# Kernel optimization log

Measured on AMD Instinct MI355X. Metric: run time of the kernel, lower is better.

The kernel has to match this reference:

```python
import jax, jax.numpy as jnp
import numpy as np

B, H, W, C = 16, 56, 56, 512
NUM_HEADS = 8
WS = 4  # window_size


def setup_inputs() -> dict:
    key = jax.random.key(0)
    k1, k2, k3, k4 = jax.random.split(key, 4)
    x = jax.random.normal(k1, (B, H, W, C), dtype=jnp.float32)
    w_qkv_h = jax.random.normal(k2, (3 * C, C), dtype=jnp.float32) * 0.02
    w_qkv_l = jax.random.normal(k3, (3 * C, C), dtype=jnp.float32) * 0.02
    w_proj = jax.random.normal(k4, (C, 2 * C), dtype=jnp.float32) * 0.02
    b_proj = jnp.zeros((C,), dtype=jnp.float32)
    return {"x": x, "w_qkv_h": w_qkv_h, "w_qkv_l": w_qkv_l,
            "w_proj": w_proj, "b_proj": b_proj}


def reference(x, w_qkv_h, w_qkv_l, w_proj, b_proj):
    b, h, w, c = x.shape
    nh = NUM_HEADS
    hd = c // nh
    nw = WS * WS  # tokens per window
    scale = c ** -0.5  # NOTE: original scales by full dim, not head dim

    # window partition: [B*H/ws*W/ws, ws*ws, C]
    xw = x.reshape(b, h // WS, WS, w // WS, WS, c)
    xw = xw.transpose(0, 1, 3, 2, 4, 5).reshape(-1, nw, c)

    # local branch qkv: [3, Nwin, nh, nw, hd]
    qkv_h = (xw @ w_qkv_h.T).reshape(-1, nw, 3, nh, hd).transpose(2, 0, 3, 1, 4)
    q_h, k_h, v_h = qkv_h[0], qkv_h[1], qkv_h[2]

    # global branch: average-pool each window to a single token [Nwin, 1, C]
    x_avg = x.reshape(b, h // WS, WS, w // WS, WS, c).mean(axis=(2, 4))
    x_avg = x_avg.reshape(-1, 1, c)
    qkv_l = (x_avg @ w_qkv_l.T).reshape(-1, 1, 3, nh, hd).transpose(2, 0, 3, 1, 4)
    q_l, k_l, v_l = qkv_l[0], qkv_l[1], qkv_l[2]

    # local window attention: [Nwin, nh, nw, nw]
    attn_h = jax.nn.softmax(jnp.einsum('bhqd,bhkd->bhqk', q_h, k_h) * scale, axis=-1)
    x_h = jnp.einsum('bhqk,bhkd->bhqd', attn_h, v_h)
    x_h = x_h.transpose(0, 2, 1, 3).reshape(-1, nw, c)

    # pooled global attention (1 token -> softmax over singleton = 1)
    attn_l = jax.nn.softmax(jnp.einsum('bhqd,bhkd->bhqk', q_l, k_l) * scale, axis=-1)
    x_l = jnp.einsum('bhqk,bhkd->bhqd', attn_l, v_l)
    x_l = x_l.transpose(0, 2, 1, 3).reshape(-1, 1, c)

    # concat local + broadcast global, project 2C -> C
    x_out = jnp.concatenate([x_h, jnp.broadcast_to(x_l, (x_l.shape[0], nw, c))], axis=-1)
    x_out = x_out @ w_proj.T + b_proj

    # window reverse
    x_out = x_out.reshape(b, h // WS, w // WS, WS, WS, c)
    x_out = x_out.transpose(0, 1, 3, 2, 4, 5).reshape(b, h, w, c)
    return x_out
```

## Files before the change

kernel.cpp:

```cpp
#include <hip/hip_runtime.h>


using bf16x8 = __attribute__((ext_vector_type(8))) short;
using f32x4  = __attribute__((ext_vector_type(4))) float;

#define SCALE 0.044194173824159216f

__device__ __forceinline__ unsigned short f2bf(float f) {
    union { float f; unsigned u; } v; v.f = f;
    unsigned u = v.u;
    return (unsigned short)((u + 0x7fffu + ((u >> 16) & 1u)) >> 16);
}

__device__ __forceinline__ void gl2lds16(const unsigned short* g, unsigned short* l) {
    __builtin_amdgcn_global_load_lds(
        (const __attribute__((address_space(1))) void*)g,
        (__attribute__((address_space(3))) void*)l, 16, 0, 0);
}

__global__ void k_prep_weights(const float* __restrict__ wqkv_h,
                               const float* __restrict__ wqkv_l,
                               const float* __restrict__ wproj,
                               unsigned short* __restrict__ WH,
                               unsigned short* __restrict__ WLV,
                               unsigned short* __restrict__ WP1,
                               unsigned short* __restrict__ WP2) {
    int i = blockIdx.x * 256 + threadIdx.x;
    if (i < 786432) {
        WH[i] = f2bf(wqkv_h[i]);
    } else {
        int j = i - 786432;
        int r = j >> 18;
        int t = j & 262143;
        int n = t >> 9, k = t & 511;
        if (r == 0)      WLV[t] = f2bf(wqkv_l[(1024 + n) * 512 + k]);
        else if (r == 1) WP1[t] = f2bf(wproj[n * 1024 + k]);
        else             WP2[t] = f2bf(wproj[n * 1024 + 512 + k]);
    }
}

__global__ void k_window_pool(const float* __restrict__ x,
                              unsigned short* __restrict__ XW,
                              unsigned short* __restrict__ XAVG) {
    int win = blockIdx.x * 2 + (threadIdx.x >> 7);
    int g = threadIdx.x & 127;
    int c = g * 4;
    int b = win / 196, rem = win % 196, wh = rem / 14, ww = rem % 14;
    float4 s = {0.f, 0.f, 0.f, 0.f};
    #pragma unroll
    for (int t = 0; t < 16; ++t) {
        int row = (b * 56 + wh * 4 + (t >> 2)) * 56 + ww * 4 + (t & 3);
        float4 v = *(const float4*)&x[(size_t)row * 512 + c];
        uint2 pk;
        pk.x = (unsigned)f2bf(v.x) | ((unsigned)f2bf(v.y) << 16);
        pk.y = (unsigned)f2bf(v.z) | ((unsigned)f2bf(v.w) << 16);
        *(uint2*)&XW[(size_t)(win * 16 + t) * 512 + c] = pk;
        s.x += v.x; s.y += v.y; s.z += v.z; s.w += v.w;
    }
    uint2 pa;
    pa.x = (unsigned)f2bf(s.x * 0.0625f) | ((unsigned)f2bf(s.y * 0.0625f) << 16);
    pa.y = (unsigned)f2bf(s.z * 0.0625f) | ((unsigned)f2bf(s.w * 0.0625f) << 16);
    *(uint2*)&XAVG[(size_t)win * 512 + c] = pa;
}

template <int NT>
__global__ void k_gemm512(const unsigned short* __restrict__ A,
                          const unsigned short* __restrict__ Bw,
                          unsigned short* __restrict__ outB,
                          float* __restrict__ outF,
                          const float* __restrict__ bias) {
    int wave = threadIdx.x >> 6, lane = threadIdx.x & 63;
    int quad = lane >> 4, l16 = lane & 15;
    int m0 = blockIdx.x * 64 + wave * 16;
    int n0 = blockIdx.y * (NT * 16);
    f32x4 acc[NT] = {};
    const unsigned short* arow = A + (size_t)(m0 + l16) * 512 + quad * 8;
    for (int kk = 0; kk < 16; ++kk) {
        bf16x8 a = *(const bf16x8*)(arow + kk * 32);
        #pragma unroll
        for (int nt = 0; nt < NT; ++nt) {
            bf16x8 b = *(const bf16x8*)(Bw + (size_t)(n0 + nt * 16 + l16) * 512 + kk * 32 + quad * 8);
            acc[nt] = __builtin_amdgcn_mfma_f32_16x16x32_bf16(a, b, acc[nt], 0, 0, 0);
        }
    }
    #pragma unroll
    for (int nt = 0; nt < NT; ++nt) {
        int col = n0 + nt * 16 + l16;
        float bv = (bias != nullptr) ? bias[col] : 0.f;
        #pragma unroll
        for (int r = 0; r < 4; ++r) {
            int row = m0 + quad * 4 + r;
            if (outF != nullptr) outF[(size_t)row * 512 + col] = acc[nt][r] + bv;
            else                 outB[(size_t)row * 512 + col] = f2bf(acc[nt][r]);
        }
    }
}

__global__ void __launch_bounds__(256, 4) k_fused(const unsigned short* __restrict__ XW,
                                                  const unsigned short* __restrict__ WH,
                                                  unsigned short* __restrict__ XH) {
    __shared__ __align__(16) char smem[33792];
    unsigned short* As  = (unsigned short*)smem;
    unsigned short* Bs  = (unsigned short*)(smem + 8192);
    unsigned short* qs  = (unsigned short*)smem;
    unsigned short* ks  = (unsigned short*)(smem + 9216);
    unsigned short* vts = (unsigned short*)(smem + 18432);
    unsigned short* Ps  = (unsigned short*)(smem + 29696);

    const int wave = threadIdx.x >> 6, lane = threadIdx.x & 63;
    const int quad = lane >> 4, l16 = lane & 15;

    int id  = blockIdx.y * 784 + blockIdx.x;
    int s   = id >> 3;
    int tb  = (id & 7) * 98 + (s >> 3);
    int head = s & 7;
    const int m0 = tb * 64;
    const int t0 = wave * 16;
    const unsigned short* Bh = WH + head * 32768;

    int aofs[2], bofs[6];
    #pragma unroll
    for (int i = 0; i < 2; ++i) {
        int u = (wave * 2 + i) * 64 + lane;
        int n = u >> 3;
        int gu = (lane & 7) ^ (n & 7);
        aofs[i] = (m0 + n) * 512 + gu * 8;
    }
    #pragma unroll
    for (int i = 0; i < 6; ++i) {
        int u = (wave * 6 + i) * 64 + lane;
        int n = u >> 3;
        int gu = (lane & 7) ^ (n & 7);
        int nrow = (n >> 6) * 512 + (n & 63);
        bofs[i] = nrow * 512 + gu * 8;
    }

    f32x4 acc[4][3] = {};
    const int sx = l16 & 7;

    for (int ch = 0; ch < 8; ++ch) {
        #pragma unroll
        for (int i = 0; i < 2; ++i)
            gl2lds16(XW + aofs[i] + ch * 64, As + (wave * 2 + i) * 512);
        #pragma unroll
        for (int i = 0; i < 6; ++i)
            gl2lds16(Bh + bofs[i] + ch * 64, Bs + (wave * 6 + i) * 512);
        __syncthreads();
        #pragma unroll
        for (int kk = 0; kk < 2; ++kk) {
            int su = ((kk * 4 + quad) ^ sx) * 8;
            bf16x8 a[4], b[3];
            #pragma unroll
            for (int mf = 0; mf < 4; ++mf)
                a[mf] = *(const bf16x8*)&As[(mf * 16 + l16) * 64 + su];
            #pragma unroll
            for (int j = 0; j < 3; ++j)
                b[j] = *(const bf16x8*)&Bs[(wave * 48 + j * 16 + l16) * 64 + su];
            #pragma unroll
            for (int mf = 0; mf < 4; ++mf)
                #pragma unroll
                for (int j = 0; j < 3; ++j)
                    acc[mf][j] = __builtin_amdgcn_mfma_f32_16x16x32_bf16(a[mf], b[j], acc[mf][j], 0, 0, 0);
        }
        __syncthreads();
    }

    #pragma unroll
    for (int j = 0; j < 3; ++j) {
        int cb = wave * 48 + j * 16;
        #pragma unroll
        for (int mf = 0; mf < 4; ++mf) {
            #pragma unroll
            for (int r = 0; r < 4; ++r) {
                int tok = mf * 16 + quad * 4 + r;
                unsigned short hv = f2bf(acc[mf][j][r]);
                if (cb < 64)       qs[tok * 72 + cb + l16] = hv;
                else if (cb < 128) ks[tok * 72 + (cb - 64) + l16] = hv;
                else               vts[(cb - 128 + l16) * 88 + tok] = hv;
            }
        }
    }
    __syncthreads();

    if (wave == 3) {
        #pragma unroll
        for (int i = 0; i < 16; ++i) vts[lane * 88 + 64 + i] = 0;
    }
    {
        int prow = lane >> 2, pc = 16 + (lane & 3) * 4;
        #pragma unroll
        for (int i = 0; i < 4; ++i) Ps[wave * 512 + prow * 32 + pc + i] = 0;
    }

    f32x4 sacc = {};
    {
        bf16x8 a0 = *(const bf16x8*)&qs[(t0 + l16) * 72 + quad * 8];
        bf16x8 b0 = *(const bf16x8*)&ks[(t0 + l16) * 72 + quad * 8];
        sacc = __builtin_amdgcn_mfma_f32_16x16x32_bf16(a0, b0, sacc, 0, 0, 0);
        bf16x8 a1 = *(const bf16x8*)&qs[(t0 + l16) * 72 + 32 + quad * 8];
        bf16x8 b1 = *(const bf16x8*)&ks[(t0 + l16) * 72 + 32 + quad * 8];
        sacc = __builtin_amdgcn_mfma_f32_16x16x32_bf16(a1, b1, sacc, 0, 0, 0);
    }
    float p[4];
    #pragma unroll
    for (int r = 0; r < 4; ++r) {
        float v = sacc[r] * SCALE;
        float m = v;
        m = fmaxf(m, __shfl_xor(m, 1));
        m = fmaxf(m, __shfl_xor(m, 2));
        m = fmaxf(m, __shfl_xor(m, 4));
        m = fmaxf(m, __shfl_xor(m, 8));
        float e = __expf(v - m);
        float sm = e;
        sm += __shfl_xor(sm, 1);
        sm += __shfl_xor(sm, 2);
        sm += __shfl_xor(sm, 4);
        sm += __shfl_xor(sm, 8);
        p[r] = e / sm;
    }
    #pragma unroll
    for (int r = 0; r < 4; ++r)
        Ps[wave * 512 + (quad * 4 + r) * 32 + l16] = f2bf(p[r]);

    bf16x8 pa = *(const bf16x8*)&Ps[wave * 512 + l16 * 32 + quad * 8];
    #pragma unroll
    for (int nt = 0; nt < 4; ++nt) {
        f32x4 y = {};
        bf16x8 bv = *(const bf16x8*)&vts[(nt * 16 + l16) * 88 + t0 + quad * 8];
        y = __builtin_amdgcn_mfma_f32_16x16x32_bf16(pa, bv, y, 0, 0, 0);
        #pragma unroll
        for (int r = 0; r < 4; ++r)
            XH[(size_t)(m0 + t0 + quad * 4 + r) * 512 + head * 64 + nt * 16 + l16] = f2bf(y[r]);
    }
}

__global__ void __launch_bounds__(256, 3) k_gemm_proj(const unsigned short* __restrict__ XH,
                                                      const unsigned short* __restrict__ WP1,
                                                      const float* __restrict__ G,
                                                      float* __restrict__ out) {
    __shared__ __align__(16) unsigned short As[8192];
    __shared__ __align__(16) unsigned short Bs[8192];

    const int wave = threadIdx.x >> 6, lane = threadIdx.x & 63;
    const int quad = lane >> 4, l16 = lane & 15;

    int id = blockIdx.y * 392 + blockIdx.x;
    int s  = id >> 3;
    int xb = (id & 7) * 49 + (s >> 2);
    int yb = s & 3;
    const int m0 = xb * 128, n0 = yb * 128;
    const int wm = (wave >> 1) * 64;
    const int wn = (wave & 1) * 64;

    int aofs[4], bofs[4];
    #pragma unroll
    for (int i = 0; i < 4; ++i) {
        int u = (wave * 4 + i) * 64 + lane;
        int n = u >> 3;
        int gu = (lane & 7) ^ (n & 7);
        aofs[i] = (m0 + n) * 512 + gu * 8;
        bofs[i] = (n0 + n) * 512 + gu * 8;
    }

    f32x4 acc[4][4] = {};
    const int sx = l16 & 7;

    for (int ch = 0; ch < 8; ++ch) {
        #pragma unroll
        for (int i = 0; i < 4; ++i) {
            gl2lds16(XH + aofs[i] + ch * 64, As + (wave * 4 + i) * 512);
            gl2lds16(WP1 + bofs[i] + ch * 64, Bs + (wave * 4 + i) * 512);
        }
        __syncthreads();
        #pragma unroll
        for (int kk = 0; kk < 2; ++kk) {
            int su = ((kk * 4 + quad) ^ sx) * 8;
            bf16x8 a[4], b[4];
            #pragma unroll
            for (int mf = 0; mf < 4; ++mf)
                a[mf] = *(const bf16x8*)&As[(wm + mf * 16 + l16) * 64 + su];
            #pragma unroll
            for (int j = 0; j < 4; ++j)
                b[j] = *(const bf16x8*)&Bs[(wn + j * 16 + l16) * 64 + su];
            #pragma unroll
            for (int mf = 0; mf < 4; ++mf)
                #pragma unroll
                for (int j = 0; j < 4; ++j)
                    acc[mf][j] = __builtin_amdgcn_mfma_f32_16x16x32_bf16(a[mf], b[j], acc[mf][j], 0, 0, 0);
        }
        __syncthreads();
    }

    #pragma unroll
    for (int mf = 0; mf < 4; ++mf) {
        #pragma unroll
        for (int r = 0; r < 4; ++r) {
            int tl  = wm + mf * 16 + quad * 4 + r;
            int gt  = m0 + tl;
            int win = gt >> 4, tw = gt & 15;
            int bb = win / 196, rem = win % 196;
            int wh = rem / 14, ww = rem % 14;
            int orow = (bb * 56 + wh * 4 + (tw >> 2)) * 56 + ww * 4 + (tw & 3);
            #pragma unroll
            for (int j = 0; j < 4; ++j) {
                int ncol = n0 + wn + j * 16 + l16;
                out[(size_t)orow * 512 + ncol] = acc[mf][j][r] + G[(size_t)win * 512 + ncol];
            }
        }
    }
}

extern "C" void kernel_launch(void* const* d_in, const int* in_sizes, int n_in,
                              void* d_out, int out_size, void* d_ws, size_t ws_size,
                              hipStream_t stream) {
    const float* x      = (const float*)d_in[0];
    const float* wqkv_h = (const float*)d_in[1];
    const float* wqkv_l = (const float*)d_in[2];
    const float* wproj  = (const float*)d_in[3];
    const float* bproj  = (const float*)d_in[4];
    float* out = (float*)d_out;

    char* ws = (char*)d_ws;
    unsigned short* WH   = (unsigned short*)(ws + 0);
    unsigned short* WLV  = (unsigned short*)(ws + 1572864);
    unsigned short* WP1  = (unsigned short*)(ws + 2097152);
    unsigned short* WP2  = (unsigned short*)(ws + 2621440);
    unsigned short* XW   = (unsigned short*)(ws + 3145728);
    unsigned short* XAVG = (unsigned short*)(ws + 54525952);
    unsigned short* VL   = (unsigned short*)(ws + 57737216);
    float*          G    = (float*)(ws + 60948480);
    unsigned short* XH   = (unsigned short*)(ws + 67371008);

    k_prep_weights<<<dim3(6144), dim3(256), 0, stream>>>(wqkv_h, wqkv_l, wproj, WH, WLV, WP1, WP2);
    k_window_pool<<<dim3(1568), dim3(256), 0, stream>>>(x, XW, XAVG);
    k_gemm512<2><<<dim3(49, 16), dim3(256), 0, stream>>>(XAVG, WLV, VL, (float*)nullptr, (const float*)nullptr);
    k_gemm512<2><<<dim3(49, 16), dim3(256), 0, stream>>>(VL, WP2, (unsigned short*)nullptr, G, bproj);
    k_fused<<<dim3(784, 8), dim3(256), 0, stream>>>(XW, WH, XH);
    k_gemm_proj<<<dim3(392, 4), dim3(256), 0, stream>>>(XH, WP1, G, out);
}
```

Baseline: 386.6 us.

## Double-buffer LDS loads in fused attention and projection GEMMs, widen fused blocks

```diff
diff --git a/kernel.cpp b/kernel.cpp
--- a/kernel.cpp
+++ b/kernel.cpp
@@ -96,66 +96,84 @@
     }
 }
 
-__global__ void __launch_bounds__(256, 4) k_fused(const unsigned short* __restrict__ XW,
+__global__ void __launch_bounds__(512, 4) k_fused(const unsigned short* __restrict__ XW,
                                                   const unsigned short* __restrict__ WH,
                                                   unsigned short* __restrict__ XH) {
-    __shared__ __align__(16) char smem[33792];
-    unsigned short* As  = (unsigned short*)smem;
-    unsigned short* Bs  = (unsigned short*)(smem + 8192);
-    unsigned short* qs  = (unsigned short*)smem;
-    unsigned short* ks  = (unsigned short*)(smem + 9216);
-    unsigned short* vts = (unsigned short*)(smem + 18432);
-    unsigned short* Ps  = (unsigned short*)(smem + 29696);
-
-    const int wave = threadIdx.x >> 6, lane = threadIdx.x & 63;
+    __shared__ __align__(16) char smem[81920];
+
+    const int tid  = threadIdx.x;
+    const int wave = tid >> 6, lane = tid & 63;
     const int quad = lane >> 4, l16 = lane & 15;
-
-    int id  = blockIdx.y * 784 + blockIdx.x;
-    int s   = id >> 3;
-    int tb  = (id & 7) * 98 + (s >> 3);
-    int head = s & 7;
-    const int m0 = tb * 64;
-    const int t0 = wave * 16;
-    const unsigned short* Bh = WH + head * 32768;
-
-    int aofs[2], bofs[6];
+    const int mh = wave >> 2, nq = wave & 3;
+
+    int id   = blockIdx.y * 392 + blockIdx.x;
+    int s_   = id >> 3;
+    int tb   = (id & 7) * 49 + (s_ >> 3);
+    int head = s_ & 7;
+    const int m0 = tb * 128;
+
+    size_t aof[2];
     #pragma unroll
     for (int i = 0; i < 2; ++i) {
-        int u = (wave * 2 + i) * 64 + lane;
+        int u = i * 512 + tid;
         int n = u >> 3;
-        int gu = (lane & 7) ^ (n & 7);
-        aofs[i] = (m0 + n) * 512 + gu * 8;
-    }
-    #pragma unroll
-    for (int i = 0; i < 6; ++i) {
-        int u = (wave * 6 + i) * 64 + lane;
+        int gu = (u & 7) ^ (n & 7);
+        aof[i] = (size_t)(m0 + n) * 512 + gu * 8;
+    }
+    size_t bof[3];
+    #pragma unroll
+    for (int i = 0; i < 3; ++i) {
+        int u = i * 512 + tid;
         int n = u >> 3;
-        int gu = (lane & 7) ^ (n & 7);
-        int nrow = (n >> 6) * 512 + (n & 63);
-        bofs[i] = nrow * 512 + gu * 8;
-    }
+        int gu = (u & 7) ^ (n & 7);
+        int nrow = (n >> 6) * 512 + head * 64 + (n & 63);
+        bof[i] = (size_t)nrow * 512 + gu * 8;
+    }
+
+    unsigned short* const bufA[2] = { (unsigned short*)smem,
+                                      (unsigned short*)(smem + 40960) };
+    unsigned short* const bufB[2] = { (unsigned short*)(smem + 16384),
+                                      (unsigned short*)(smem + 40960 + 16384) };
 
     f32x4 acc[4][3] = {};
     const int sx = l16 & 7;
 
+    #pragma unroll
+    for (int i = 0; i < 2; ++i)
+        gl2lds16(XW + aof[i], bufA[0] + (i * 512 + wave * 64) * 8);
+    #pragma unroll
+    for (int i = 0; i < 3; ++i)
+        gl2lds16(WH + bof[i], bufB[0] + (i * 512 + wave * 64) * 8);
+    __syncthreads();
+
+    #pragma unroll
     for (int ch = 0; ch < 8; ++ch) {
-        #pragma unroll
-        for (int i = 0; i < 2; ++i)
-            gl2lds16(XW + aofs[i] + ch * 64, As + (wave * 2 + i) * 512);
-        #pragma unroll
-        for (int i = 0; i < 6; ++i)
-            gl2lds16(Bh + bofs[i] + ch * 64, Bs + (wave * 6 + i) * 512);
-        __syncthreads();
+        unsigned short* As = bufA[ch & 1];
+        unsigned short* Bs = bufB[ch & 1];
+        if (ch < 7) {
+            unsigned short* An = bufA[(ch + 1) & 1];
+            unsigned short* Bn = bufB[(ch + 1) & 1];
+            #pragma unroll
+            for (int i = 0; i < 2; ++i)
+                gl2lds16(XW + aof[i] + (ch + 1) * 64, An + (i * 512 + wave * 64) * 8);
+            #pragma unroll
+            for (int i = 0; i < 3; ++i)
+                gl2lds16(WH + bof[i] + (ch + 1) * 64, Bn + (i * 512 + wave * 64) * 8);
+        }
         #pragma unroll
         for (int kk = 0; kk < 2; ++kk) {
             int su = ((kk * 4 + quad) ^ sx) * 8;
             bf16x8 a[4], b[3];
             #pragma unroll
-            for (int mf = 0; mf < 4; ++mf)
-                a[mf] = *(const bf16x8*)&As[(mf * 16 + l16) * 64 + su];
-            #pragma unroll
-            for (int j = 0; j < 3; ++j)
-                b[j] = *(const bf16x8*)&Bs[(wave * 48 + j * 16 + l16) * 64 + su];
+            for (int mf = 0; mf < 4; ++mf) {
+                int row = mh * 64 + mf * 16 + l16;
+                a[mf] = *(const bf16x8*)&As[row * 64 + (((kk * 4 + quad) ^ (row & 7)) ^ sx ^ (row & 7)) * 8];
+            }
+            #pragma unroll
+            for (int j = 0; j < 3; ++j) {
+                int brow = nq * 48 + j * 16 + l16;
+                b[j] = *(const bf16x8*)&Bs[brow * 64 + (((kk * 4 + quad) ^ (brow & 7)) ^ sx ^ (brow & 7)) * 8];
+            }
             #pragma unroll
             for (int mf = 0; mf < 4; ++mf)
                 #pragma unroll
@@ -165,31 +183,44 @@
         __syncthreads();
     }
 
-    #pragma unroll
-    for (int j = 0; j < 3; ++j) {
-        int cb = wave * 48 + j * 16;
-        #pragma unroll
-        for (int mf = 0; mf < 4; ++mf) {
-            #pragma unroll
-            for (int r = 0; r < 4; ++r) {
-                int tok = mf * 16 + quad * 4 + r;
-                unsigned short hv = f2bf(acc[mf][j][r]);
-                if (cb < 64)       qs[tok * 72 + cb + l16] = hv;
-                else if (cb < 128) ks[tok * 72 + (cb - 64) + l16] = hv;
-                else               vts[(cb - 128 + l16) * 88 + tok] = hv;
+    {
+        char* att = smem + mh * 33792;
+        unsigned short* qs  = (unsigned short*)att;
+        unsigned short* ks  = (unsigned short*)(att + 9216);
+        unsigned short* vts = (unsigned short*)(att + 18432);
+        #pragma unroll
+        for (int j = 0; j < 3; ++j) {
+            int cb = nq * 48 + j * 16;
+            #pragma unroll
+            for (int mf = 0; mf < 4; ++mf) {
+                #pragma unroll
+                for (int r = 0; r < 4; ++r) {
+                    int tok = mf * 16 + quad * 4 + r;
+                    unsigned short hv = f2bf(acc[mf][j][r]);
+                    if (cb < 64)       qs[tok * 72 + cb + l16] = hv;
+                    else if (cb < 128) ks[tok * 72 + (cb - 64) + l16] = hv;
+                    else               vts[(cb - 128 + l16) * 88 + tok] = hv;
+                }
             }
         }
     }
     __syncthreads();
 
-    if (wave == 3) {
+    char* att = smem + (wave >> 2) * 33792;
+    unsigned short* qs  = (unsigned short*)att;
+    unsigned short* ks  = (unsigned short*)(att + 9216);
+    unsigned short* vts = (unsigned short*)(att + 18432);
+    unsigned short* Ps  = (unsigned short*)(att + 29696);
+    const int lw = wave & 3, t0 = lw * 16;
+
+    if (lw == 3) {
         #pragma unroll
         for (int i = 0; i < 16; ++i) vts[lane * 88 + 64 + i] = 0;
     }
     {
         int prow = lane >> 2, pc = 16 + (lane & 3) * 4;
         #pragma unroll
-        for (int i = 0; i < 4; ++i) Ps[wave * 512 + prow * 32 + pc + i] = 0;
+        for (int i = 0; i < 4; ++i) Ps[lw * 512 + prow * 32 + pc + i] = 0;
     }
 
     f32x4 sacc = {};
@@ -220,9 +251,9 @@
     }
     #pragma unroll
     for (int r = 0; r < 4; ++r)
-        Ps[wave * 512 + (quad * 4 + r) * 32 + l16] = f2bf(p[r]);
-
-    bf16x8 pa = *(const bf16x8*)&Ps[wave * 512 + l16 * 32 + quad * 8];
+        Ps[lw * 512 + (quad * 4 + r) * 32 + l16] = f2bf(p[r]);
+
+    bf16x8 pa = *(const bf16x8*)&Ps[lw * 512 + l16 * 32 + quad * 8];
     #pragma unroll
     for (int nt = 0; nt < 4; ++nt) {
         f32x4 y = {};
@@ -230,16 +261,15 @@
         y = __builtin_amdgcn_mfma_f32_16x16x32_bf16(pa, bv, y, 0, 0, 0);
         #pragma unroll
         for (int r = 0; r < 4; ++r)
-            XH[(size_t)(m0 + t0 + quad * 4 + r) * 512 + head * 64 + nt * 16 + l16] = f2bf(y[r]);
-    }
-}
-
-__global__ void __launch_bounds__(256, 3) k_gemm_proj(const unsigned short* __restrict__ XH,
+            XH[(size_t)(m0 + (wave >> 2) * 64 + t0 + quad * 4 + r) * 512 + head * 64 + nt * 16 + l16] = f2bf(y[r]);
+    }
+}
+
+__global__ void __launch_bounds__(256, 2) k_gemm_proj(const unsigned short* __restrict__ XH,
                                                       const unsigned short* __restrict__ WP1,
                                                       const float* __restrict__ G,
                                                       float* __restrict__ out) {
-    __shared__ __align__(16) unsigned short As[8192];
-    __shared__ __align__(16) unsigned short Bs[8192];
+    __shared__ __align__(16) char smem[65536];
 
     const int wave = threadIdx.x >> 6, lane = threadIdx.x & 63;
     const int quad = lane >> 4, l16 = lane & 15;
@@ -252,26 +282,44 @@
     const int wm = (wave >> 1) * 64;
     const int wn = (wave & 1) * 64;
 
-    int aofs[4], bofs[4];
+    size_t aofs[4], bofs[4];
     #pragma unroll
     for (int i = 0; i < 4; ++i) {
         int u = (wave * 4 + i) * 64 + lane;
         int n = u >> 3;
         int gu = (lane & 7) ^ (n & 7);
-        aofs[i] = (m0 + n) * 512 + gu * 8;
-        bofs[i] = (n0 + n) * 512 + gu * 8;
-    }
+        aofs[i] = (size_t)(m0 + n) * 512 + gu * 8;
+        bofs[i] = (size_t)(n0 + n) * 512 + gu * 8;
+    }
+
+    unsigned short* const bufA[2] = { (unsigned short*)smem,
+                                      (unsigned short*)(smem + 32768) };
+    unsigned short* const bufB[2] = { (unsigned short*)(smem + 16384),
+                                      (unsigned short*)(smem + 32768 + 16384) };
 
     f32x4 acc[4][4] = {};
     const int sx = l16 & 7;
 
+    #pragma unroll
+    for (int i = 0; i < 4; ++i) {
+        gl2lds16(XH + aofs[i], bufA[0] + (wave * 4 + i) * 512);
+        gl2lds16(WP1 + bofs[i], bufB[0] + (wave * 4 + i) * 512);
+    }
+    __syncthreads();
+
+    #pragma unroll
     for (int ch = 0; ch < 8; ++ch) {
-        #pragma unroll
-        for (int i = 0; i < 4; ++i) {
-            gl2lds16(XH + aofs[i] + ch * 64, As + (wave * 4 + i) * 512);
-            gl2lds16(WP1 + bofs[i] + ch * 64, Bs + (wave * 4 + i) * 512);
-        }
-        __syncthreads();
+        unsigned short* As = bufA[ch & 1];
+        unsigned short* Bs = bufB[ch & 1];
+        if (ch < 7) {
+            unsigned short* An = bufA[(ch + 1) & 1];
+            unsigned short* Bn = bufB[(ch + 1) & 1];
+            #pragma unroll
+            for (int i = 0; i < 4; ++i) {
+                gl2lds16(XH + aofs[i] + (ch + 1) * 64, An + (wave * 4 + i) * 512);
+                gl2lds16(WP1 + bofs[i] + (ch + 1) * 64, Bn + (wave * 4 + i) * 512);
+            }
+        }
         #pragma unroll
         for (int kk = 0; kk < 2; ++kk) {
             int su = ((kk * 4 + quad) ^ sx) * 8;
@@ -335,6 +383,6 @@
     k_window_pool<<<dim3(1568), dim3(256), 0, stream>>>(x, XW, XAVG);
     k_gemm512<2><<<dim3(49, 16), dim3(256), 0, stream>>>(XAVG, WLV, VL, (float*)nullptr, (const float*)nullptr);
     k_gemm512<2><<<dim3(49, 16), dim3(256), 0, stream>>>(VL, WP2, (unsigned short*)nullptr, G, bproj);
-    k_fused<<<dim3(784, 8), dim3(256), 0, stream>>>(XW, WH, XH);
+    k_fused<<<dim3(392, 8), dim3(512), 0, stream>>>(XW, WH, XH);
     k_gemm_proj<<<dim3(392, 4), dim3(256), 0, stream>>>(XH, WP1, G, out);
 }
```

After: 392.5 us. About the same (+1.5%).
